# Performance work log

Hardware: AMD Instinct MI355X
Metric: run time of the kernel (lower is better)

## Reference

```python
import jax, jax.numpy as jnp
import numpy as np

N_NODES = 100000
N_EDGES = 1600000
DIM_IN, DIM_H, DIM_OUT = 64, 128, 8


def _glorot(key, shape):
    fan_in, fan_out = shape
    lim = jnp.sqrt(6.0 / (fan_in + fan_out))
    return jax.random.uniform(key, shape, jnp.float32, -lim, lim)


def setup_inputs() -> dict:
    key = jax.random.key(0)
    ks = jax.random.split(key, 16)
    x = jax.random.normal(ks[0], (N_NODES, DIM_IN), jnp.float32)
    edge_index = jax.random.randint(ks[1], (2, N_EDGES), 0, N_NODES, jnp.int64 if jax.config.jax_enable_x64 else jnp.int32)
    dims = [(DIM_IN, DIM_H), (DIM_H, DIM_H), (DIM_H, 1), (1, DIM_OUT)]
    inp = {"x": x, "edge_index": edge_index}
    for i, (di, do) in enumerate(dims, start=1):
        inp[f"W{i}l"] = _glorot(ks[2 + 3 * (i - 1)], (di, do))
        inp[f"W{i}r"] = _glorot(ks[3 + 3 * (i - 1)], (di, do))
        inp[f"b{i}"] = jnp.zeros((do,), jnp.float32)
    return inp


def _sage_conv(x, src, dst, Wl, Wr, b):
    # mean aggregation over in-edges (PyG SAGEConv default):
    # out = lin_l(mean_{j in N(i)} x_j) + lin_r(x_i)
    agg = jax.ops.segment_sum(x[src], dst, num_segments=N_NODES)  # [N, d]
    cnt = jax.ops.segment_sum(jnp.ones((src.shape[0],), x.dtype), dst, num_segments=N_NODES)
    mean = agg / jnp.maximum(cnt, 1.0)[:, None]
    return mean @ Wl + x @ Wr + b


def reference(x, edge_index, W1l, W1r, b1, W2l, W2r, b2, W3l, W3r, b3, W4l, W4r, b4):
    src, dst = edge_index[0], edge_index[1]
    h = jax.nn.relu(_sage_conv(x, src, dst, W1l, W1r, b1))
    h = jax.nn.relu(_sage_conv(h, src, dst, W2l, W2r, b2))
    h = _sage_conv(h, src, dst, W3l, W3r, b3)          # [N, 1]
    out_scalar_field = h[:, 0]                          # [N]
    h = _sage_conv(h, src, dst, W4l, W4r, b4)           # [N, dim_out]
    out_rock_unit = jax.nn.log_softmax(h, axis=1)
    return (out_rock_unit, out_scalar_field)
```

## Files before the change

### kernel.cpp

```cpp
#include <hip/hip_runtime.h>
#include <hip/hip_bf16.h>
#include <math.h>


typedef unsigned short u16;
typedef unsigned int u32;
typedef __attribute__((ext_vector_type(4))) float f32x4;
typedef __attribute__((ext_vector_type(8))) short s16x8;

__device__ __forceinline__ float b2f(u16 u) {
  union { float f; u32 i; } v; v.i = ((u32)u) << 16; return v.f;
}
__device__ __forceinline__ u16 f2b(float f) {
  union { float f; u32 u; } v; v.f = f;
  u32 r = v.u + 0x7fffu + ((v.u >> 16) & 1u);
  return (u16)(r >> 16);
}

__global__ __launch_bounds__(512) void bucket_hist(const int* __restrict__ ei,
                                                   int* __restrict__ gbh, int E) {
  __shared__ int hist[1024];
  const int t = threadIdx.x;
  const int base = blockIdx.x * 8192;
  const int cnt = min(8192, E - base);
  for (int b = t; b < 1024; b += 512) hist[b] = 0;
  __syncthreads();
  for (int k = t; k < cnt; k += 512)
    atomicAdd(&hist[ei[E + base + k] >> 7], 1);
  __syncthreads();
  for (int b = t; b < 1024; b += 512)
    gbh[blockIdx.x * 1024 + b] = hist[b];
}

__global__ __launch_bounds__(512) void scan_buckets(const int* __restrict__ gbh,
                                                    int nblk,
                                                    int* __restrict__ bucket_base,
                                                    int* __restrict__ gcur,
                                                    int* __restrict__ rowptr,
                                                    int N, int E) {
  __shared__ int wsum[512];
  const int t = threadIdx.x;
  int c0 = 0, c1 = 0;
  for (int blk = 0; blk < nblk; ++blk) {
    c0 += gbh[blk * 1024 + 2 * t];
    c1 += gbh[blk * 1024 + 2 * t + 1];
  }
  int s = c0 + c1;
  wsum[t] = s;
  __syncthreads();
  for (int off = 1; off < 512; off <<= 1) {
    int add = (t >= off) ? wsum[t - off] : 0;
    __syncthreads();
    wsum[t] += add;
    __syncthreads();
  }
  int excl = wsum[t] - s;
  bucket_base[2 * t] = excl;
  bucket_base[2 * t + 1] = excl + c0;
  gcur[2 * t] = excl;
  gcur[2 * t + 1] = excl + c0;
  if (t == 511) bucket_base[1024] = wsum[511];
  if (t == 0) rowptr[N] = E;
}

__global__ __launch_bounds__(512) void bucketize(const int* __restrict__ ei,
                                                 int* __restrict__ gcur,
                                                 u32* __restrict__ staging,
                                                 int E, int B) {
  __shared__ u32 vals[8192];
  __shared__ u16 bkt[8192];
  __shared__ int hist[1024], ofs[1024], curx[1024], gbase[1024];
  __shared__ int wsum[512];

  const int t = threadIdx.x;
  const int base = blockIdx.x * 8192;
  const int cnt = min(8192, E - base);

  for (int b = t; b < 1024; b += 512) hist[b] = 0;
  __syncthreads();

  for (int k = t; k < cnt; k += 512) {
    int d = ei[E + base + k];
    atomicAdd(&hist[d >> 7], 1);
  }
  __syncthreads();

  int a0 = hist[2 * t], a1 = hist[2 * t + 1];
  int s = a0 + a1;
  wsum[t] = s;
  __syncthreads();
  for (int off = 1; off < 512; off <<= 1) {
    int add = (t >= off) ? wsum[t - off] : 0;
    __syncthreads();
    wsum[t] += add;
    __syncthreads();
  }
  int excl = wsum[t] - s;
  ofs[2 * t] = excl;
  ofs[2 * t + 1] = excl + a0;
  __syncthreads();

  for (int b = t; b < B; b += 512) {
    int c = hist[b];
    gbase[b] = c ? atomicAdd(&gcur[b], c) : 0;
    curx[b] = ofs[b];
  }
  __syncthreads();

  for (int k = t; k < cnt; k += 512) {
    int sv = ei[base + k];
    int d = ei[E + base + k];
    int b = d >> 7;
    u32 val = (u32)sv | ((u32)(d & 127) << 17);
    int lpos = atomicAdd(&curx[b], 1);
    vals[lpos] = val;
    bkt[lpos] = (u16)b;
  }
  __syncthreads();

  for (int i = t; i < cnt; i += 512) {
    int b = bkt[i];
    staging[gbase[b] + (i - ofs[b])] = vals[i];
  }
}

__global__ __launch_bounds__(256) void place(const u32* __restrict__ staging,
                                             const int* __restrict__ bucket_base,
                                             int* __restrict__ rowptr,
                                             int* __restrict__ csr, int N) {
  __shared__ int cnt[128], excl[128], cur[128], sc[128];
  const int t = threadIdx.x;
  const int node0 = blockIdx.x << 7;
  const int nn = min(128, N - node0);
  if (t < 128) { cnt[t] = 0; cur[t] = 0; }
  __syncthreads();
  const int rstart = bucket_base[blockIdx.x];
  const int rend = bucket_base[blockIdx.x + 1];
  for (int i = rstart + t; i < rend; i += 256)
    atomicAdd(&cnt[staging[i] >> 17], 1);
  __syncthreads();
  if (t < 128) sc[t] = cnt[t];
  __syncthreads();
  for (int off = 1; off < 128; off <<= 1) {
    int add = (t < 128 && t >= off) ? sc[t - off] : 0;
    __syncthreads();
    if (t < 128) sc[t] += add;
    __syncthreads();
  }
  if (t < 128) excl[t] = sc[t] - cnt[t];
  if (t < nn) rowptr[node0 + t] = rstart + excl[t];
  __syncthreads();
  for (int i = rstart + t; i < rend; i += 256) {
    u32 v = staging[i];
    int nl = v >> 17;
    int src = v & 0x1FFFF;
    int tk = atomicAdd(&cur[nl], 1);
    csr[rstart + excl[nl] + tk] = src;
  }
}

__global__ __launch_bounds__(256) void cvt_x(const float* __restrict__ x,
                                             u16* __restrict__ xb, int total4) {
  int i = blockIdx.x * 256 + threadIdx.x;
  if (i >= total4) return;
  float4 v = *(const float4*)(x + (size_t)i * 4);
  u32 lo = (u32)f2b(v.x) | ((u32)f2b(v.y) << 16);
  u32 hi = (u32)f2b(v.z) | ((u32)f2b(v.w) << 16);
  uint2 o; o.x = lo; o.y = hi;
  *(uint2*)(xb + (size_t)i * 4) = o;
}

__global__ __launch_bounds__(256) void cvt_w(const float* __restrict__ W1l,
                                             const float* __restrict__ W1r,
                                             const float* __restrict__ W2l,
                                             const float* __restrict__ W2r,
                                             u16* __restrict__ wt1,
                                             u16* __restrict__ wt2) {
  int i = blockIdx.x * 256 + threadIdx.x;
  if (i < 16384) {
    int j = i >> 7, k = i & 127;
    float v = (k < 64) ? W1l[k * 128 + j] : W1r[(k - 64) * 128 + j];
    wt1[j * 128 + k] = f2b(v);
  } else if (i < 16384 + 32768) {
    int i2 = i - 16384;
    int j = i2 >> 8, k = i2 & 255;
    float v = (k < 128) ? W2l[k * 128 + j] : W2r[(k - 128) * 128 + j];
    wt2[j * 256 + k] = f2b(v);
  }
}

#define ACC8(v)                                                        \
  a0 += b2f((u16)(v).x); a1 += b2f((u16)((v).x >> 16));                \
  a2 += b2f((u16)(v).y); a3 += b2f((u16)((v).y >> 16));                \
  a4 += b2f((u16)(v).z); a5 += b2f((u16)((v).z >> 16));                \
  a6 += b2f((u16)(v).w); a7 += b2f((u16)((v).w >> 16));

__global__ __launch_bounds__(256) void gather_mean_64b(const u16* __restrict__ xb,
                                                       const int* __restrict__ rowptr,
                                                       const int* __restrict__ csr,
                                                       u16* __restrict__ mean, int N) {
  int n = (blockIdx.x * 256 + threadIdx.x) >> 6;
  int lane = threadIdx.x & 63;
  int sub = lane >> 3;
  int ln = lane & 7;
  if (n >= N) return;
  int s0 = rowptr[n], s1 = rowptr[n + 1];
  float a0 = 0.f, a1 = 0.f, a2 = 0.f, a3 = 0.f, a4 = 0.f, a5 = 0.f, a6 = 0.f, a7 = 0.f;
  int e = s0;
  for (; e + 16 <= s1; e += 16) {
    int i0 = csr[e + sub], i1 = csr[e + 8 + sub];
    uint4 v0 = *(const uint4*)(xb + (size_t)i0 * 64 + ln * 8);
    uint4 v1 = *(const uint4*)(xb + (size_t)i1 * 64 + ln * 8);
    ACC8(v0); ACC8(v1);
  }
  for (; e + 8 <= s1; e += 8) {
    int i0 = csr[e + sub];
    uint4 v0 = *(const uint4*)(xb + (size_t)i0 * 64 + ln * 8);
    ACC8(v0);
  }
  int rem = s1 - e;
  if (sub < rem) {
    int i0 = csr[e + sub];
    uint4 v0 = *(const uint4*)(xb + (size_t)i0 * 64 + ln * 8);
    ACC8(v0);
  }
#pragma unroll
  for (int off = 8; off < 64; off <<= 1) {
    a0 += __shfl_xor(a0, off); a1 += __shfl_xor(a1, off);
    a2 += __shfl_xor(a2, off); a3 += __shfl_xor(a3, off);
    a4 += __shfl_xor(a4, off); a5 += __shfl_xor(a5, off);
    a6 += __shfl_xor(a6, off); a7 += __shfl_xor(a7, off);
  }
  if (sub == 0) {
    int c = s1 - s0;
    float inv = c > 0 ? 1.f / (float)c : 0.f;
    uint4 o;
    o.x = (u32)f2b(a0 * inv) | ((u32)f2b(a1 * inv) << 16);
    o.y = (u32)f2b(a2 * inv) | ((u32)f2b(a3 * inv) << 16);
    o.z = (u32)f2b(a4 * inv) | ((u32)f2b(a5 * inv) << 16);
    o.w = (u32)f2b(a6 * inv) | ((u32)f2b(a7 * inv) << 16);
    *(uint4*)(mean + (size_t)n * 64 + ln * 8) = o;
  }
}

__global__ __launch_bounds__(256) void gather_mean_128b(const u16* __restrict__ hb,
                                                        const int* __restrict__ rowptr,
                                                        const int* __restrict__ csr,
                                                        u16* __restrict__ mean, int N) {
  int n = (blockIdx.x * 256 + threadIdx.x) >> 6;
  int lane = threadIdx.x & 63;
  int sub = lane >> 4;
  int ln = lane & 15;
  if (n >= N) return;
  int s0 = rowptr[n], s1 = rowptr[n + 1];
  float a0 = 0.f, a1 = 0.f, a2 = 0.f, a3 = 0.f, a4 = 0.f, a5 = 0.f, a6 = 0.f, a7 = 0.f;
  int e = s0;
  for (; e + 8 <= s1; e += 8) {
    int i0 = csr[e + sub], i1 = csr[e + 4 + sub];
    uint4 v0 = *(const uint4*)(hb + (size_t)i0 * 128 + ln * 8);
    uint4 v1 = *(const uint4*)(hb + (size_t)i1 * 128 + ln * 8);
    ACC8(v0); ACC8(v1);
  }
  for (; e + 4 <= s1; e += 4) {
    int i0 = csr[e + sub];
    uint4 v0 = *(const uint4*)(hb + (size_t)i0 * 128 + ln * 8);
    ACC8(v0);
  }
  int rem = s1 - e;
  if (sub < rem) {
    int i0 = csr[e + sub];
    uint4 v0 = *(const uint4*)(hb + (size_t)i0 * 128 + ln * 8);
    ACC8(v0);
  }
#pragma unroll
  for (int off = 16; off < 64; off <<= 1) {
    a0 += __shfl_xor(a0, off); a1 += __shfl_xor(a1, off);
    a2 += __shfl_xor(a2, off); a3 += __shfl_xor(a3, off);
    a4 += __shfl_xor(a4, off); a5 += __shfl_xor(a5, off);
    a6 += __shfl_xor(a6, off); a7 += __shfl_xor(a7, off);
  }
  if (sub == 0) {
    int c = s1 - s0;
    float inv = c > 0 ? 1.f / (float)c : 0.f;
    uint4 o;
    o.x = (u32)f2b(a0 * inv) | ((u32)f2b(a1 * inv) << 16);
    o.y = (u32)f2b(a2 * inv) | ((u32)f2b(a3 * inv) << 16);
    o.z = (u32)f2b(a4 * inv) | ((u32)f2b(a5 * inv) << 16);
    o.w = (u32)f2b(a6 * inv) | ((u32)f2b(a7 * inv) << 16);
    *(uint4*)(mean + (size_t)n * 128 + ln * 8) = o;
  }
}

template<int K2, bool FINAL>
__global__ __launch_bounds__(512) void mfma_gemm(
    const u16* __restrict__ meanb, const u16* __restrict__ prevb,
    const u16* __restrict__ wt,
    const float* __restrict__ bias,
    u16* __restrict__ hout,
    const float* __restrict__ W3l, const float* __restrict__ W3r,
    float* __restrict__ outp, float* __restrict__ outq, int N) {
  constexpr int KH = K2 / 2;
  constexpr int NC = K2 / 8;
  __shared__ __align__(16) u16 Albs[128 * K2];
  __shared__ __align__(16) u16 Wlds[128 * K2];

  const int t = threadIdx.x;
  const int tile = blockIdx.x * 128;

  for (int i = t; i < 128 * NC; i += 512) {
    int j = i / NC, c = i - j * NC;
    uint4 v = *(const uint4*)(wt + (size_t)j * K2 + c * 8);
    *(uint4*)(Wlds + j * K2 + ((c ^ (j & 7)) << 3)) = v;
  }
  for (int i = t; i < 128 * NC; i += 512) {
    int r = i / NC, c = i - r * NC;
    int node = tile + r;
    uint4 v; v.x = 0; v.y = 0; v.z = 0; v.w = 0;
    if (node < N) {
      int k0 = c * 8;
      v = (k0 < KH) ? *(const uint4*)(meanb + (size_t)node * KH + k0)
                    : *(const uint4*)(prevb + (size_t)node * KH + (k0 - KH));
    }
    *(uint4*)(Albs + r * K2 + ((c ^ (r & 7)) << 3)) = v;
  }
  __syncthreads();

  const int lane = t & 63;
  const int wid = t >> 6;
  const int wm = wid >> 1, wn = wid & 1;
  const int er = lane & 15;
  const int kg = lane >> 4;

  f32x4 acc[2][4];
#pragma unroll
  for (int mi = 0; mi < 2; ++mi)
#pragma unroll
    for (int ni = 0; ni < 4; ++ni) acc[mi][ni] = (f32x4)(0.f);

#pragma unroll
  for (int ks = 0; ks < K2 / 32; ++ks) {
    int cidx = ks * 4 + kg;
    s16x8 a[2], b[4];
#pragma unroll
    for (int mi = 0; mi < 2; ++mi) {
      int row = wm * 32 + mi * 16 + er;
      a[mi] = *(const s16x8*)(Albs + row * K2 + ((cidx ^ (row & 7)) << 3));
    }
#pragma unroll
    for (int ni = 0; ni < 4; ++ni) {
      int col = wn * 64 + ni * 16 + er;
      b[ni] = *(const s16x8*)(Wlds + col * K2 + ((cidx ^ (col & 7)) << 3));
    }
#pragma unroll
    for (int mi = 0; mi < 2; ++mi)
#pragma unroll
      for (int ni = 0; ni < 4; ++ni)
        acc[mi][ni] = __builtin_amdgcn_mfma_f32_16x16x32_bf16(a[mi], b[ni], acc[mi][ni], 0, 0, 0);
  }

  if constexpr (!FINAL) {
#pragma unroll
    for (int mi = 0; mi < 2; ++mi) {
#pragma unroll
      for (int ni = 0; ni < 4; ++ni) {
        int col = wn * 64 + ni * 16 + er;
        float bv = bias[col];
#pragma unroll
        for (int r = 0; r < 4; ++r) {
          int node = tile + wm * 32 + mi * 16 + kg * 4 + r;
          if (node < N) {
            float v = acc[mi][ni][r] + bv;
            v = v > 0.f ? v : 0.f;
            hout[(size_t)node * 128 + col] = f2b(v);
          }
        }
      }
    }
  } else {
    __shared__ float p_lds[128][2], q_lds[128][2];
    float wl[4], wr[4], bv[4];
#pragma unroll
    for (int ni = 0; ni < 4; ++ni) {
      int col = wn * 64 + ni * 16 + er;
      wl[ni] = W3l[col]; wr[ni] = W3r[col]; bv[ni] = bias[col];
    }
#pragma unroll
    for (int mi = 0; mi < 2; ++mi) {
#pragma unroll
      for (int r = 0; r < 4; ++r) {
        float pv = 0.f, qv = 0.f;
#pragma unroll
        for (int ni = 0; ni < 4; ++ni) {
          float v = acc[mi][ni][r] + bv[ni];
          v = v > 0.f ? v : 0.f;
          pv = fmaf(v, wl[ni], pv);
          qv = fmaf(v, wr[ni], qv);
        }
#pragma unroll
        for (int off = 1; off < 16; off <<= 1) {
          pv += __shfl_xor(pv, off);
          qv += __shfl_xor(qv, off);
        }
        if (er == 0) {
          int nl = wm * 32 + mi * 16 + kg * 4 + r;
          p_lds[nl][wn] = pv;
          q_lds[nl][wn] = qv;
        }
      }
    }
    __syncthreads();
    if (t < 128) {
      int node = tile + t;
      if (node < N) {
        outp[node] = p_lds[t][0] + p_lds[t][1];
        outq[node] = q_lds[t][0] + q_lds[t][1];
      }
    }
  }
}

__global__ __launch_bounds__(256) void gather3_fused(const float* __restrict__ p,
                                                     const int* __restrict__ rowptr,
                                                     const int* __restrict__ csr,
                                                     const float* __restrict__ q,
                                                     const float* __restrict__ b3,
                                                     float* __restrict__ h3,
                                                     float* __restrict__ out_scalar, int N) {
  int n = blockIdx.x * 256 + threadIdx.x;
  if (n >= N) return;
  int s0 = rowptr[n], s1 = rowptr[n + 1];
  float a = 0.f;
  for (int e = s0; e < s1; ++e) a += p[csr[e]];
  int c = s1 - s0;
  float inv = c > 0 ? 1.f / (float)c : 0.f;
  float v = a * inv + q[n] + b3[0];
  h3[n] = v;
  out_scalar[n] = v;
}

__global__ __launch_bounds__(256) void gather4_fused(const float* __restrict__ h3,
                                                     const int* __restrict__ rowptr,
                                                     const int* __restrict__ csr,
                                                     const float* __restrict__ W4l,
                                                     const float* __restrict__ W4r,
                                                     const float* __restrict__ b4,
                                                     float* __restrict__ out, int N) {
  int n = blockIdx.x * 256 + threadIdx.x;
  if (n >= N) return;
  int s0 = rowptr[n], s1 = rowptr[n + 1];
  float a = 0.f;
  for (int e = s0; e < s1; ++e) a += h3[csr[e]];
  int c = s1 - s0;
  float inv = c > 0 ? 1.f / (float)c : 0.f;
  float m = a * inv;
  float hv = h3[n];
  float logits[8];
  float mx = -1e30f;
#pragma unroll
  for (int jj = 0; jj < 8; ++jj) {
    float v = m * W4l[jj] + hv * W4r[jj] + b4[jj];
    logits[jj] = v;
    mx = v > mx ? v : mx;
  }
  float s = 0.f;
#pragma unroll
  for (int jj = 0; jj < 8; ++jj) s += expf(logits[jj] - mx);
  float lse = mx + logf(s);
  float4 o0, o1;
  o0.x = logits[0] - lse; o0.y = logits[1] - lse; o0.z = logits[2] - lse; o0.w = logits[3] - lse;
  o1.x = logits[4] - lse; o1.y = logits[5] - lse; o1.z = logits[6] - lse; o1.w = logits[7] - lse;
  float4* o4 = (float4*)(out + (size_t)n * 8);
  o4[0] = o0; o4[1] = o1;
}

extern "C" void kernel_launch(void* const* d_in, const int* in_sizes, int n_in,
                              void* d_out, int out_size, void* d_ws, size_t ws_size,
                              hipStream_t stream) {
  const float* x   = (const float*)d_in[0];
  const int*   ei  = (const int*)d_in[1];
  const float* W1l = (const float*)d_in[2];
  const float* W1r = (const float*)d_in[3];
  const float* b1  = (const float*)d_in[4];
  const float* W2l = (const float*)d_in[5];
  const float* W2r = (const float*)d_in[6];
  const float* b2  = (const float*)d_in[7];
  const float* W3l = (const float*)d_in[8];
  const float* W3r = (const float*)d_in[9];
  const float* b3  = (const float*)d_in[10];
  const float* W4l = (const float*)d_in[11];
  const float* W4r = (const float*)d_in[12];
  const float* b4  = (const float*)d_in[13];

  const int N = in_sizes[0] / 64;
  const int E = in_sizes[1] / 2;
  const size_t Ns = (size_t)N;
  const int B = (N + 127) >> 7;
  const int NBLK = (E + 8191) / 8192;

  u16* ub      = (u16*)d_ws;
  u16* xb      = ub;
  u16* mean0b  = ub + 64 * Ns;
  u16* h1b     = ub + 128 * Ns;
  u16* mean1b  = ub + 256 * Ns;
  u16* wt1     = ub + 384 * Ns;
  u16* wt2     = wt1 + 16384;
  float* fb    = (float*)(wt2 + 32768);
  float* p     = fb;
  float* q     = fb + Ns;
  float* h3    = fb + 2 * Ns;
  int* ib      = (int*)(fb + 3 * Ns);
  int* rowptr      = ib;
  int* gcur        = ib + (N + 1);
  int* bucket_base = gcur + 1024;
  int* gbh         = bucket_base + 1025;
  int* csr         = gbh + NBLK * 1024;
  u32* staging     = (u32*)(csr + E);

  float* out_rock   = (float*)d_out;
  float* out_scalar = (float*)d_out + 8 * Ns;

  const int GG = (N + 127) / 128;

  bucket_hist<<<NBLK, 512, 0, stream>>>(ei, gbh, E);
  scan_buckets<<<1, 512, 0, stream>>>(gbh, NBLK, bucket_base, gcur, rowptr, N, E);
  bucketize<<<NBLK, 512, 0, stream>>>(ei, gcur, staging, E, B);
  place<<<B, 256, 0, stream>>>(staging, bucket_base, rowptr, csr, N);

  cvt_x<<<(N * 16 + 255) / 256, 256, 0, stream>>>(x, xb, N * 16);
  cvt_w<<<192, 256, 0, stream>>>(W1l, W1r, W2l, W2r, wt1, wt2);

  gather_mean_64b<<<(N + 3) / 4, 256, 0, stream>>>(xb, rowptr, csr, mean0b, N);
  mfma_gemm<128, false><<<GG, 512, 0, stream>>>(
      mean0b, xb, wt1, b1, h1b, nullptr, nullptr, nullptr, nullptr, N);

  gather_mean_128b<<<(N + 3) / 4, 256, 0, stream>>>(h1b, rowptr, csr, mean1b, N);
  mfma_gemm<256, true><<<GG, 512, 0, stream>>>(
      mean1b, h1b, wt2, b2, nullptr, W3l, W3r, p, q, N);

  gather3_fused<<<(N + 255) / 256, 256, 0, stream>>>(p, rowptr, csr, q, b3, h3, out_scalar, N);

  gather4_fused<<<(N + 255) / 256, 256, 0, stream>>>(h3, rowptr, csr, W4l, W4r, b4, out_rock, N);
}
```

Before: 260.8 us.

## Streamline CSR build, merge conversion kernels, and pack bf16 accumulation

```diff
diff --git a/kernel.cpp b/kernel.cpp
--- a/kernel.cpp
+++ b/kernel.cpp
@@ -5,6 +5,7 @@
 
 typedef unsigned short u16;
 typedef unsigned int u32;
+typedef __attribute__((ext_vector_type(2))) float f32x2;
 typedef __attribute__((ext_vector_type(4))) float f32x4;
 typedef __attribute__((ext_vector_type(8))) short s16x8;
 
@@ -16,9 +17,17 @@
   u32 r = v.u + 0x7fffu + ((v.u >> 16) & 1u);
   return (u16)(r >> 16);
 }
+__device__ __forceinline__ f32x2 up2(u32 v) {
+  union { float f; u32 u; } lo, hi;
+  lo.u = v << 16;
+  hi.u = v & 0xFFFF0000u;
+  f32x2 r; r.x = lo.f; r.y = hi.f; return r;
+}
 
 __global__ __launch_bounds__(512) void bucket_hist(const int* __restrict__ ei,
-                                                   int* __restrict__ gbh, int E) {
+                                                   int* __restrict__ gbh,
+                                                   int* __restrict__ bucket_count,
+                                                   int E) {
   __shared__ int hist[1024];
   const int t = threadIdx.x;
   const int base = blockIdx.x * 8192;
@@ -28,23 +37,22 @@
   for (int k = t; k < cnt; k += 512)
     atomicAdd(&hist[ei[E + base + k] >> 7], 1);
   __syncthreads();
-  for (int b = t; b < 1024; b += 512)
-    gbh[blockIdx.x * 1024 + b] = hist[b];
-}
-
-__global__ __launch_bounds__(512) void scan_buckets(const int* __restrict__ gbh,
-                                                    int nblk,
-                                                    int* __restrict__ bucket_base,
-                                                    int* __restrict__ gcur,
-                                                    int* __restrict__ rowptr,
-                                                    int N, int E) {
+  for (int b = t; b < 1024; b += 512) {
+    int c = hist[b];
+    gbh[blockIdx.x * 1024 + b] = c;
+    if (c) atomicAdd(&bucket_count[b], c);
+  }
+}
+
+__global__ __launch_bounds__(512) void scan_tiny(const int* __restrict__ bucket_count,
+                                                 int* __restrict__ bucket_base,
+                                                 int* __restrict__ gcur,
+                                                 int* __restrict__ rowptr,
+                                                 int N, int E) {
   __shared__ int wsum[512];
   const int t = threadIdx.x;
-  int c0 = 0, c1 = 0;
-  for (int blk = 0; blk < nblk; ++blk) {
-    c0 += gbh[blk * 1024 + 2 * t];
-    c1 += gbh[blk * 1024 + 2 * t + 1];
-  }
+  int c0 = bucket_count[2 * t];
+  int c1 = bucket_count[2 * t + 1];
   int s = c0 + c1;
   wsum[t] = s;
   __syncthreads();
@@ -64,6 +72,7 @@
 }
 
 __global__ __launch_bounds__(512) void bucketize(const int* __restrict__ ei,
+                                                 const int* __restrict__ gbh,
                                                  int* __restrict__ gcur,
                                                  u32* __restrict__ staging,
                                                  int E, int B) {
@@ -76,13 +85,7 @@
   const int base = blockIdx.x * 8192;
   const int cnt = min(8192, E - base);
 
-  for (int b = t; b < 1024; b += 512) hist[b] = 0;
-  __syncthreads();
-
-  for (int k = t; k < cnt; k += 512) {
-    int d = ei[E + base + k];
-    atomicAdd(&hist[d >> 7], 1);
-  }
+  for (int b = t; b < 1024; b += 512) hist[b] = gbh[blockIdx.x * 1024 + b];
   __syncthreads();
 
   int a0 = hist[2 * t], a1 = hist[2 * t + 1];
@@ -159,41 +162,38 @@
   }
 }
 
-__global__ __launch_bounds__(256) void cvt_x(const float* __restrict__ x,
-                                             u16* __restrict__ xb, int total4) {
+__global__ __launch_bounds__(256) void cvt_all(const float* __restrict__ x,
+                                               u16* __restrict__ xb, int total4,
+                                               const float* __restrict__ W1l,
+                                               const float* __restrict__ W1r,
+                                               const float* __restrict__ W2l,
+                                               const float* __restrict__ W2r,
+                                               u16* __restrict__ wt1,
+                                               u16* __restrict__ wt2) {
   int i = blockIdx.x * 256 + threadIdx.x;
-  if (i >= total4) return;
-  float4 v = *(const float4*)(x + (size_t)i * 4);
-  u32 lo = (u32)f2b(v.x) | ((u32)f2b(v.y) << 16);
-  u32 hi = (u32)f2b(v.z) | ((u32)f2b(v.w) << 16);
-  uint2 o; o.x = lo; o.y = hi;
-  *(uint2*)(xb + (size_t)i * 4) = o;
-}
-
-__global__ __launch_bounds__(256) void cvt_w(const float* __restrict__ W1l,
-                                             const float* __restrict__ W1r,
-                                             const float* __restrict__ W2l,
-                                             const float* __restrict__ W2r,
-                                             u16* __restrict__ wt1,
-                                             u16* __restrict__ wt2) {
-  int i = blockIdx.x * 256 + threadIdx.x;
-  if (i < 16384) {
-    int j = i >> 7, k = i & 127;
-    float v = (k < 64) ? W1l[k * 128 + j] : W1r[(k - 64) * 128 + j];
-    wt1[j * 128 + k] = f2b(v);
-  } else if (i < 16384 + 32768) {
-    int i2 = i - 16384;
-    int j = i2 >> 8, k = i2 & 255;
-    float v = (k < 128) ? W2l[k * 128 + j] : W2r[(k - 128) * 128 + j];
-    wt2[j * 256 + k] = f2b(v);
-  }
-}
-
-#define ACC8(v)                                                        \
-  a0 += b2f((u16)(v).x); a1 += b2f((u16)((v).x >> 16));                \
-  a2 += b2f((u16)(v).y); a3 += b2f((u16)((v).y >> 16));                \
-  a4 += b2f((u16)(v).z); a5 += b2f((u16)((v).z >> 16));                \
-  a6 += b2f((u16)(v).w); a7 += b2f((u16)((v).w >> 16));
+  if (i < total4) {
+    float4 v = *(const float4*)(x + (size_t)i * 4);
+    u32 lo = (u32)f2b(v.x) | ((u32)f2b(v.y) << 16);
+    u32 hi = (u32)f2b(v.z) | ((u32)f2b(v.w) << 16);
+    uint2 o; o.x = lo; o.y = hi;
+    *(uint2*)(xb + (size_t)i * 4) = o;
+    return;
+  }
+  int j = i - total4;
+  if (j < 16384) {
+    int jj = j >> 7, k = j & 127;
+    float v = (k < 64) ? W1l[k * 128 + jj] : W1r[(k - 64) * 128 + jj];
+    wt1[jj * 128 + k] = f2b(v);
+  } else if (j < 16384 + 32768) {
+    int i2 = j - 16384;
+    int jj = i2 >> 8, k = i2 & 255;
+    float v = (k < 128) ? W2l[k * 128 + jj] : W2r[(k - 128) * 128 + jj];
+    wt2[jj * 256 + k] = f2b(v);
+  }
+}
+
+#define PACC(v)                                                        \
+  a0 += up2((v).x); a1 += up2((v).y); a2 += up2((v).z); a3 += up2((v).w);
 
 __global__ __launch_bounds__(256) void gather_mean_64b(const u16* __restrict__ xb,
                                                        const int* __restrict__ rowptr,
@@ -205,40 +205,40 @@
   int ln = lane & 7;
   if (n >= N) return;
   int s0 = rowptr[n], s1 = rowptr[n + 1];
-  float a0 = 0.f, a1 = 0.f, a2 = 0.f, a3 = 0.f, a4 = 0.f, a5 = 0.f, a6 = 0.f, a7 = 0.f;
+  f32x2 a0 = (f32x2)(0.f), a1 = (f32x2)(0.f), a2 = (f32x2)(0.f), a3 = (f32x2)(0.f);
   int e = s0;
   for (; e + 16 <= s1; e += 16) {
     int i0 = csr[e + sub], i1 = csr[e + 8 + sub];
     uint4 v0 = *(const uint4*)(xb + (size_t)i0 * 64 + ln * 8);
     uint4 v1 = *(const uint4*)(xb + (size_t)i1 * 64 + ln * 8);
-    ACC8(v0); ACC8(v1);
+    PACC(v0); PACC(v1);
   }
   for (; e + 8 <= s1; e += 8) {
     int i0 = csr[e + sub];
     uint4 v0 = *(const uint4*)(xb + (size_t)i0 * 64 + ln * 8);
-    ACC8(v0);
+    PACC(v0);
   }
   int rem = s1 - e;
   if (sub < rem) {
     int i0 = csr[e + sub];
     uint4 v0 = *(const uint4*)(xb + (size_t)i0 * 64 + ln * 8);
-    ACC8(v0);
+    PACC(v0);
   }
 #pragma unroll
   for (int off = 8; off < 64; off <<= 1) {
-    a0 += __shfl_xor(a0, off); a1 += __shfl_xor(a1, off);
-    a2 += __shfl_xor(a2, off); a3 += __shfl_xor(a3, off);
-    a4 += __shfl_xor(a4, off); a5 += __shfl_xor(a5, off);
-    a6 += __shfl_xor(a6, off); a7 += __shfl_xor(a7, off);
+    a0.x += __shfl_xor(a0.x, off); a0.y += __shfl_xor(a0.y, off);
+    a1.x += __shfl_xor(a1.x, off); a1.y += __shfl_xor(a1.y, off);
+    a2.x += __shfl_xor(a2.x, off); a2.y += __shfl_xor(a2.y, off);
+    a3.x += __shfl_xor(a3.x, off); a3.y += __shfl_xor(a3.y, off);
   }
   if (sub == 0) {
     int c = s1 - s0;
     float inv = c > 0 ? 1.f / (float)c : 0.f;
     uint4 o;
-    o.x = (u32)f2b(a0 * inv) | ((u32)f2b(a1 * inv) << 16);
-    o.y = (u32)f2b(a2 * inv) | ((u32)f2b(a3 * inv) << 16);
-    o.z = (u32)f2b(a4 * inv) | ((u32)f2b(a5 * inv) << 16);
-    o.w = (u32)f2b(a6 * inv) | ((u32)f2b(a7 * inv) << 16);
+    o.x = (u32)f2b(a0.x * inv) | ((u32)f2b(a0.y * inv) << 16);
+    o.y = (u32)f2b(a1.x * inv) | ((u32)f2b(a1.y * inv) << 16);
+    o.z = (u32)f2b(a2.x * inv) | ((u32)f2b(a2.y * inv) << 16);
+    o.w = (u32)f2b(a3.x * inv) | ((u32)f2b(a3.y * inv) << 16);
     *(uint4*)(mean + (size_t)n * 64 + ln * 8) = o;
   }
 }
@@ -253,40 +253,40 @@
   int ln = lane & 15;
   if (n >= N) return;
   int s0 = rowptr[n], s1 = rowptr[n + 1];
-  float a0 = 0.f, a1 = 0.f, a2 = 0.f, a3 = 0.f, a4 = 0.f, a5 = 0.f, a6 = 0.f, a7 = 0.f;
+  f32x2 a0 = (f32x2)(0.f), a1 = (f32x2)(0.f), a2 = (f32x2)(0.f), a3 = (f32x2)(0.f);
   int e = s0;
   for (; e + 8 <= s1; e += 8) {
     int i0 = csr[e + sub], i1 = csr[e + 4 + sub];
     uint4 v0 = *(const uint4*)(hb + (size_t)i0 * 128 + ln * 8);
     uint4 v1 = *(const uint4*)(hb + (size_t)i1 * 128 + ln * 8);
-    ACC8(v0); ACC8(v1);
+    PACC(v0); PACC(v1);
   }
   for (; e + 4 <= s1; e += 4) {
     int i0 = csr[e + sub];
     uint4 v0 = *(const uint4*)(hb + (size_t)i0 * 128 + ln * 8);
-    ACC8(v0);
+    PACC(v0);
   }
   int rem = s1 - e;
   if (sub < rem) {
     int i0 = csr[e + sub];
     uint4 v0 = *(const uint4*)(hb + (size_t)i0 * 128 + ln * 8);
-    ACC8(v0);
+    PACC(v0);
   }
 #pragma unroll
   for (int off = 16; off < 64; off <<= 1) {
-    a0 += __shfl_xor(a0, off); a1 += __shfl_xor(a1, off);
-    a2 += __shfl_xor(a2, off); a3 += __shfl_xor(a3, off);
-    a4 += __shfl_xor(a4, off); a5 += __shfl_xor(a5, off);
-    a6 += __shfl_xor(a6, off); a7 += __shfl_xor(a7, off);
+    a0.x += __shfl_xor(a0.x, off); a0.y += __shfl_xor(a0.y, off);
+    a1.x += __shfl_xor(a1.x, off); a1.y += __shfl_xor(a1.y, off);
+    a2.x += __shfl_xor(a2.x, off); a2.y += __shfl_xor(a2.y, off);
+    a3.x += __shfl_xor(a3.x, off); a3.y += __shfl_xor(a3.y, off);
   }
   if (sub == 0) {
     int c = s1 - s0;
     float inv = c > 0 ? 1.f / (float)c : 0.f;
     uint4 o;
-    o.x = (u32)f2b(a0 * inv) | ((u32)f2b(a1 * inv) << 16);
-    o.y = (u32)f2b(a2 * inv) | ((u32)f2b(a3 * inv) << 16);
-    o.z = (u32)f2b(a4 * inv) | ((u32)f2b(a5 * inv) << 16);
-    o.w = (u32)f2b(a6 * inv) | ((u32)f2b(a7 * inv) << 16);
+    o.x = (u32)f2b(a0.x * inv) | ((u32)f2b(a0.y * inv) << 16);
+    o.y = (u32)f2b(a1.x * inv) | ((u32)f2b(a1.y * inv) << 16);
+    o.z = (u32)f2b(a2.x * inv) | ((u32)f2b(a2.y * inv) << 16);
+    o.w = (u32)f2b(a3.x * inv) | ((u32)f2b(a3.y * inv) << 16);
     *(uint4*)(mean + (size_t)n * 128 + ln * 8) = o;
   }
 }
@@ -509,25 +509,28 @@
   float* q     = fb + Ns;
   float* h3    = fb + 2 * Ns;
   int* ib      = (int*)(fb + 3 * Ns);
-  int* rowptr      = ib;
-  int* gcur        = ib + (N + 1);
-  int* bucket_base = gcur + 1024;
-  int* gbh         = bucket_base + 1025;
-  int* csr         = gbh + NBLK * 1024;
-  u32* staging     = (u32*)(csr + E);
+  int* rowptr       = ib;
+  int* gcur         = ib + (N + 1);
+  int* bucket_base  = gcur + 1024;
+  int* bucket_count = bucket_base + 1025;
+  int* gbh          = bucket_count + 1024;
+  int* csr          = gbh + NBLK * 1024;
+  u32* staging      = (u32*)(csr + E);
 
   float* out_rock   = (float*)d_out;
   float* out_scalar = (float*)d_out + 8 * Ns;
 
   const int GG = (N + 127) / 128;
-
-  bucket_hist<<<NBLK, 512, 0, stream>>>(ei, gbh, E);
-  scan_buckets<<<1, 512, 0, stream>>>(gbh, NBLK, bucket_base, gcur, rowptr, N, E);
-  bucketize<<<NBLK, 512, 0, stream>>>(ei, gcur, staging, E, B);
+  const int total4 = N * 16;
+
+  hipMemsetAsync(bucket_count, 0, 1024 * sizeof(int), stream);
+  bucket_hist<<<NBLK, 512, 0, stream>>>(ei, gbh, bucket_count, E);
+  scan_tiny<<<1, 512, 0, stream>>>(bucket_count, bucket_base, gcur, rowptr, N, E);
+  bucketize<<<NBLK, 512, 0, stream>>>(ei, gbh, gcur, staging, E, B);
   place<<<B, 256, 0, stream>>>(staging, bucket_base, rowptr, csr, N);
 
-  cvt_x<<<(N * 16 + 255) / 256, 256, 0, stream>>>(x, xb, N * 16);
-  cvt_w<<<192, 256, 0, stream>>>(W1l, W1r, W2l, W2r, wt1, wt2);
+  cvt_all<<<(total4 + 49152 + 255) / 256, 256, 0, stream>>>(
+      x, xb, total4, W1l, W1r, W2l, W2r, wt1, wt2);
 
   gather_mean_64b<<<(N + 3) / 4, 256, 0, stream>>>(xb, rowptr, csr, mean0b, N);
   mfma_gemm<128, false><<<GG, 512, 0, stream>>>(
```

Result: faster. 240.0 us (-8.0%).
